# Optimization experiments

Hardware: AMD Instinct MI355X
Metric: run time of the kernel (lower is better)

Reference implementation:

```python
import jax, jax.numpy as jnp
import numpy as np

# Dims: batch B, seq L, embed D, router hidden H, num_blocks NB, top_k K
B, L, D, H, NB, K = 8, 4096, 1024, 64, 16, 2
TEMP = 2.0          # current_temperature buffer (init 2.0), clamp(min=0.1) inert
LN_EPS = 1e-5


def setup_inputs() -> dict:
    key = jax.random.key(0)
    k_x, k_w1, k_w2 = jax.random.split(key, 3)
    return {
        "x": jax.random.normal(k_x, (B, L, D), dtype=jnp.float32),
        "ln_gamma": jnp.ones((D,), dtype=jnp.float32),
        "ln_beta": jnp.zeros((D,), dtype=jnp.float32),
        "W1": jax.random.normal(k_w1, (D, H), dtype=jnp.float32) / np.sqrt(D).astype(np.float32),
        "W2": jax.random.normal(k_w2, (H, NB), dtype=jnp.float32) / np.sqrt(H).astype(np.float32),
    }


def reference(x, ln_gamma, ln_beta, W1, W2):
    # gate: LayerNorm -> Linear(no bias) -> GELU(exact) -> Linear(no bias)
    mu = jnp.mean(x, axis=-1, keepdims=True)
    var = jnp.mean(jnp.square(x - mu), axis=-1, keepdims=True)
    xn = (x - mu) * jax.lax.rsqrt(var + LN_EPS) * ln_gamma + ln_beta
    h = jax.nn.gelu(xn @ W1, approximate=False)          # (B, L, H)
    logits = (h @ W2) / TEMP                              # (B, L, NB)

    probs = jax.nn.softmax(logits, axis=-1)               # (B, L, NB)
    top_probs, indices = jax.lax.top_k(probs, K)          # (B, L, K) each
    weights = top_probs / (jnp.sum(top_probs, axis=-1, keepdims=True) + 1e-8)

    # load-balancing aux loss: f = fraction of assignments per block (detached),
    # P = mean router prob per block
    counts = jnp.zeros((NB,), dtype=probs.dtype).at[indices.reshape(-1)].add(1.0)
    f = jax.lax.stop_gradient(counts) / (B * L * K + 1e-8)
    P = jnp.mean(probs, axis=(0, 1))                      # (NB,)
    aux_loss = NB * jnp.sum(f * P)

    return probs, indices, aux_loss, weights
```

## Files before the change

### kernel.cpp

```cpp
#include <hip/hip_runtime.h>
#include <math.h>

typedef __attribute__((ext_vector_type(8))) short short8;
typedef __attribute__((ext_vector_type(4))) float f32x4;

#define NTOK 32768
#define DDIM 1024
#define HDIM 64
#define NB 16
#define LN_EPS 1e-5f

#define IDX_OFF ((size_t)NTOK * NB)
#define AUX_OFF (IDX_OFF + (size_t)NTOK * 2)
#define WT_OFF  (AUX_OFF + 1)

#define CS_F   64
#define BP_F   4352
#define PART_F 102656

__device__ __forceinline__ short8 as_s8(uint4 u) {
    union { uint4 u; short8 s; } x; x.u = u; return x.s;
}

__device__ __forceinline__ f32x4 ntload4(const float* p) {
    return __builtin_nontemporal_load((const f32x4*)p);
}

__device__ __forceinline__ void gld16(const unsigned int* g, float* l) {
    __builtin_amdgcn_global_load_lds(
        (const __attribute__((address_space(1))) void*)g,
        (__attribute__((address_space(3))) void*)l, 16, 0, 0);
}

__global__ void pack_kernel(const float* __restrict__ W1,
                            const float* __restrict__ gamma,
                            const float* __restrict__ beta,
                            float* __restrict__ ws) {
    __shared__ float sg[4][64];
    __shared__ float sb[4][64];
    const int s = blockIdx.x;
    const int t = threadIdx.x;

    {
        const int j = t & 63, p = t >> 6;
        float ag = 0.f, ab = 0.f;
        for (int kk = 0; kk < 8; ++kk) {
            const int k = s * 32 + p * 8 + kk;
            const float w = W1[k * HDIM + j];
            ag += gamma[k] * w;
            ab += beta[k] * w;
        }
        sg[p][j] = ag;
        sb[p][j] = ab;
    }

    {
        unsigned int* bp = (unsigned int*)(ws + BP_F);
        const int n = t >> 6;
        const int l = t & 63;
        const int q = l >> 4, c = l & 15;
        const int col = n * 16 + c;
        unsigned int uh[8], um[8], ul[8];
#pragma unroll
        for (int j = 0; j < 8; ++j) {
            const int k = s * 32 + q * 8 + j;
            const float w = gamma[k] * W1[k * HDIM + col];
            const unsigned int hb = __float_as_uint(w) & 0xFFFF0000u;
            const float r = w - __uint_as_float(hb);
            const unsigned int mb = __float_as_uint(r) & 0xFFFF0000u;
            const float r2 = r - __uint_as_float(mb);
            const unsigned int lb = __float_as_uint(r2) & 0xFFFF0000u;
            uh[j] = hb >> 16; um[j] = mb >> 16; ul[j] = lb >> 16;
        }
        const int base = ((s * 4 + n) * 64 + l) * 4;
#pragma unroll
        for (int d = 0; d < 4; ++d) {
            bp[base + d]         = uh[2 * d] | (uh[2 * d + 1] << 16);
            bp[32768 + base + d] = um[2 * d] | (um[2 * d + 1] << 16);
            bp[65536 + base + d] = ul[2 * d] | (ul[2 * d + 1] << 16);
        }
    }
    __syncthreads();
    if (t < 64) {
        atomicAdd(&ws[CS_F + t],      sg[0][t] + sg[1][t] + sg[2][t] + sg[3][t]);
        atomicAdd(&ws[CS_F + 64 + t], sb[0][t] + sb[1][t] + sb[2][t] + sb[3][t]);
    }
}

__device__ __forceinline__ void split8(const f32x4 a0, const f32x4 a1,
                                       short8& AH, short8& AM, short8& AL,
                                       float& s1, float& s2) {
    const float v[8] = {a0.x, a0.y, a0.z, a0.w, a1.x, a1.y, a1.z, a1.w};
    unsigned int ph[4], pm[4], pl[4];
#pragma unroll
    for (int d = 0; d < 4; ++d) {
        const float v0 = v[2 * d], v1 = v[2 * d + 1];
        const unsigned int h0 = __float_as_uint(v0) & 0xFFFF0000u;
        const unsigned int h1 = __float_as_uint(v1) & 0xFFFF0000u;
        const float r0 = v0 - __uint_as_float(h0);
        const float r1 = v1 - __uint_as_float(h1);
        const unsigned int m0 = __float_as_uint(r0) & 0xFFFF0000u;
        const unsigned int m1 = __float_as_uint(r1) & 0xFFFF0000u;
        const float q0 = r0 - __uint_as_float(m0);
        const float q1 = r1 - __uint_as_float(m1);
        ph[d] = (h0 >> 16) | h1;
        pm[d] = (m0 >> 16) | m1;
        pl[d] = (__float_as_uint(q0) >> 16) | (__float_as_uint(q1) & 0xFFFF0000u);
        s1 += v0 + v1;
        s2 = fmaf(v0, v0, fmaf(v1, v1, s2));
    }
    AH = as_s8(make_uint4(ph[0], ph[1], ph[2], ph[3]));
    AM = as_s8(make_uint4(pm[0], pm[1], pm[2], pm[3]));
    AL = as_s8(make_uint4(pl[0], pl[1], pl[2], pl[3]));
}

#define MFMA6(ACC, AH, AM, AL, BH, BM, BL)                                        \
    ACC = __builtin_amdgcn_mfma_f32_16x16x32_bf16(AH, as_s8(BH), ACC, 0, 0, 0);   \
    ACC = __builtin_amdgcn_mfma_f32_16x16x32_bf16(AH, as_s8(BM), ACC, 0, 0, 0);   \
    ACC = __builtin_amdgcn_mfma_f32_16x16x32_bf16(AM, as_s8(BH), ACC, 0, 0, 0);   \
    ACC = __builtin_amdgcn_mfma_f32_16x16x32_bf16(AH, as_s8(BL), ACC, 0, 0, 0);   \
    ACC = __builtin_amdgcn_mfma_f32_16x16x32_bf16(AM, as_s8(BM), ACC, 0, 0, 0);   \
    ACC = __builtin_amdgcn_mfma_f32_16x16x32_bf16(AL, as_s8(BH), ACC, 0, 0, 0);

#define STEP(S, CUR, NXT, DOSTAGE)                                               \
    {                                                                            \
        if (DOSTAGE) {                                                           \
            _Pragma("unroll")                                                    \
            for (int i = 0; i < 3; ++i) {                                        \
                const int idx = wv * 3 + i;                                      \
                const int term = idx >> 2, nn = idx & 3;                         \
                gld16(bp + term * 32768 + ((S) + 1) * 1024 + nn * 256 + lane * 4,\
                      (NXT) + term * 1024 + nn * 256);                           \
            }                                                                    \
        }                                                                        \
        const int off = (((S) + 2) & 31) * 32;                                   \
        const f32x4 p00 = ntload4(xr0 + off), p01 = ntload4(xr0 + off + 4);      \
        short8 AH0, AM0, AL0;                                                    \
        split8(a00, a01, AH0, AM0, AL0, s1a, s2a);                               \
        _Pragma("unroll")                                                        \
        for (int n = 0; n < 4; ++n) {                                            \
            const uint4 bh = *(const uint4*)((CUR) + n * 256 + lane * 4);        \
            const uint4 bm = *(const uint4*)((CUR) + 1024 + n * 256 + lane * 4); \
            const uint4 bl = *(const uint4*)((CUR) + 2048 + n * 256 + lane * 4); \
            MFMA6(acc[n], AH0, AM0, AL0, bh, bm, bl);                            \
        }                                                                        \
        a00 = b00; a01 = b01; b00 = p00; b01 = p01;                              \
        __syncthreads();                                                         \
    }

__global__ __launch_bounds__(256, 2)
void router_main(const float* __restrict__ x,
                 const float* __restrict__ ws_ro,
                 const unsigned int* __restrict__ bp,
                 const float* __restrict__ W2,
                 float* __restrict__ part,
                 float* __restrict__ out) {
    __shared__ __align__(16) float smem[10320];
    float* bstage = smem;
    float* hlds   = smem + 6144;
    float* cntl   = smem + 10304;
    float* w2l    = smem;
    float* llds   = smem + 1024;

    const int t    = threadIdx.x;
    const int wv   = t >> 6;
    const int lane = t & 63;
    const int q = lane >> 4, c = lane & 15;
    const int tok0 = blockIdx.x * 64;
    const int tokw = tok0 + wv * 16;

    if (t < 16) cntl[t] = 0.f;

    float csg[4], csb[4];
#pragma unroll
    for (int n = 0; n < 4; ++n) {
        csg[n] = ws_ro[CS_F + n * 16 + c];
        csb[n] = ws_ro[CS_F + 64 + n * 16 + c];
    }

    const float* xr0 = x + (size_t)(tokw + c) * DDIM + q * 8;

    float* const bufA = bstage;
    float* const bufB = bstage + 3072;

    {
#pragma unroll
        for (int i = 0; i < 3; ++i) {
            const int idx = wv * 3 + i;
            const int term = idx >> 2, nn = idx & 3;
            gld16(bp + term * 32768 + nn * 256 + lane * 4,
                  bufA + term * 1024 + nn * 256);
        }
    }

    f32x4 acc[4] = {{0.f,0.f,0.f,0.f},{0.f,0.f,0.f,0.f},{0.f,0.f,0.f,0.f},{0.f,0.f,0.f,0.f}};
    float s1a = 0.f, s2a = 0.f;

    f32x4 a00 = ntload4(xr0),      a01 = ntload4(xr0 + 4);
    f32x4 b00 = ntload4(xr0 + 32), b01 = ntload4(xr0 + 36);

    __syncthreads();

#pragma unroll 1
    for (int s2i = 0; s2i < 16; ++s2i) {
        const int s = s2i * 2;
        STEP(s,     bufA, bufB, 1)
        STEP(s + 1, bufB, bufA, (s2i < 15))
    }

    s1a += __shfl_xor(s1a, 16, 64); s1a += __shfl_xor(s1a, 32, 64);
    s2a += __shfl_xor(s2a, 16, 64); s2a += __shfl_xor(s2a, 32, 64);

    *(float4*)(w2l + t * 4) = *(const float4*)(W2 + t * 4);

    {
        float* hw = hlds + wv * 1040;
#pragma unroll
        for (int r = 0; r < 4; ++r) {
            const int tt = q * 4 + r;
            const float S1A = __shfl(s1a, tt, 64), S2A = __shfl(s2a, tt, 64);
            const float muA = S1A * (1.0f / 1024.0f);
            const float rsA = 1.0f / sqrtf(S2A * (1.0f / 1024.0f) - muA * muA + LN_EPS);
#pragma unroll
            for (int n = 0; n < 4; ++n) {
                const float preA = rsA * (acc[n][r] - muA * csg[n]) + csb[n];
                hw[tt * 65 + n * 16 + c] =
                    0.5f * preA * (1.0f + erff(preA * 0.70710678118654752f));
            }
        }
    }
    __syncthreads();

    {
        const int m2 = t >> 2, o = (t & 3) * 4;
        const float* hrow = hlds + (m2 >> 4) * 1040 + (m2 & 15) * 65;
        f32x4 L0 = {0.f, 0.f, 0.f, 0.f};
#pragma unroll 8
        for (int j = 0; j < 64; ++j) {
            L0 += *(const f32x4*)(w2l + j * 16 + o) * hrow[j];
        }
        *(f32x4*)(llds + m2 * 20 + o) = L0 * 0.5f;
    }
    __syncthreads();

    if (t < 64) {
        float p[16];
        float mx = -1e30f;
#pragma unroll
        for (int i = 0; i < NB; ++i) { p[i] = llds[t * 20 + i]; mx = fmaxf(mx, p[i]); }
        float ssum = 0.f;
#pragma unroll
        for (int i = 0; i < NB; ++i) { p[i] = expf(p[i] - mx); ssum += p[i]; }
        const float inv = 1.0f / ssum;
#pragma unroll
        for (int i = 0; i < NB; ++i) { p[i] *= inv; llds[t * 20 + i] = p[i]; }

        float* po = out + (size_t)(tok0 + t) * NB;
#pragma unroll
        for (int u = 0; u < 4; ++u) {
            float4 v; v.x = p[u*4]; v.y = p[u*4+1]; v.z = p[u*4+2]; v.w = p[u*4+3];
            *(float4*)(po + u * 4) = v;
        }

        float b0 = -1.f, b1 = -1.f;
        int i0 = 0, i1 = 0;
#pragma unroll
        for (int i = 0; i < NB; ++i) {
            if (p[i] > b0)      { b1 = b0; i1 = i0; b0 = p[i]; i0 = i; }
            else if (p[i] > b1) { b1 = p[i]; i1 = i; }
        }
        const float wsum = b0 + b1 + 1e-8f;
        out[IDX_OFF + (size_t)(tok0 + t) * 2]     = (float)i0;
        out[IDX_OFF + (size_t)(tok0 + t) * 2 + 1] = (float)i1;
        out[WT_OFF + (size_t)(tok0 + t) * 2]      = b0 / wsum;
        out[WT_OFF + (size_t)(tok0 + t) * 2 + 1]  = b1 / wsum;
        atomicAdd(&cntl[i0], 1.0f);
        atomicAdd(&cntl[i1], 1.0f);
    }
    __syncthreads();

    if (t < 16) {
        float ps = 0.f;
        for (int m = 0; m < 64; ++m) ps += llds[m * 20 + t];
        part[(size_t)blockIdx.x * 32 + t]      = cntl[t];
        part[(size_t)blockIdx.x * 32 + 16 + t] = ps;
    }
}

__global__ void aux_kernel(const float* __restrict__ part,
                           float* __restrict__ gacc,
                           float* __restrict__ out) {
    __shared__ float red[8][32];
    __shared__ float flag;
    const int t = threadIdx.x;
    const int b = blockIdx.x;
    const int i = t & 31, rr = t >> 5;
    const int r0 = b * 16 + rr;
    red[rr][i] = part[(size_t)r0 * 32 + i] + part[(size_t)(r0 + 8) * 32 + i];
    __syncthreads();
    if (t < 32) {
        float tot = 0.f;
#pragma unroll
        for (int p = 0; p < 8; ++p) tot += red[p][t];
        atomicAdd(&gacc[t], tot);
    }
    __syncthreads();
    if (t == 0) {
        __threadfence();
        const unsigned int old = atomicAdd((unsigned int*)(gacc + 32), 1u);
        flag = (old == 31u) ? 1.f : 0.f;
    }
    __syncthreads();
    if (flag != 0.f) {
        if (t < 32) red[0][t] = atomicAdd(&gacc[t], 0.0f);
        __syncthreads();
        if (t == 0) {
            float a = 0.f;
            for (int k = 0; k < NB; ++k) {
                const float f = red[0][k] / (65536.0f + 1e-8f);
                const float P = red[0][16 + k] * (1.0f / 32768.0f);
                a += f * P;
            }
            out[AUX_OFF] = 16.0f * a;
        }
    }
}

extern "C" void kernel_launch(void* const* d_in, const int* in_sizes, int n_in,
                              void* d_out, int out_size, void* d_ws, size_t ws_size,
                              hipStream_t stream) {
    const float* x     = (const float*)d_in[0];
    const float* gamma = (const float*)d_in[1];
    const float* beta  = (const float*)d_in[2];
    const float* W1    = (const float*)d_in[3];
    const float* W2    = (const float*)d_in[4];
    float* out = (float*)d_out;
    float* ws  = (float*)d_ws;

    (void)hipMemsetAsync(ws, 0, 192 * sizeof(float), stream);
    pack_kernel<<<32, 256, 0, stream>>>(W1, gamma, beta, ws);
    router_main<<<NTOK / 64, 256, 0, stream>>>(x, ws, (const unsigned int*)(ws + BP_F),
                                               W2, ws + PART_F, out);
    aux_kernel<<<32, 256, 0, stream>>>(ws + PART_F, ws, out);
}
```

Baseline: 227.6 us.

## Stage x through LDS with async loads, double-buffer 64-wide chunks, 128-token blocks

The main router kernel now fetches the x tiles with global_load_lds into double-buffered shared memory alongside the split W1 operands, instead of nontemporal register loads. Each barrier now covers two K-steps instead of one. Waits are explicit vmcnt counts so the next chunk's loads overlap the current MFMAs. Blocks grow to 512 threads and 128 tokens, and the aux reduction grid is halved to match. This trades more LDS per block (about 112KB, which may limit residency) for fewer barriers and better latency hiding.

```diff
diff --git a/kernel.cpp b/kernel.cpp
--- a/kernel.cpp
+++ b/kernel.cpp
@@ -22,11 +22,7 @@
     union { uint4 u; short8 s; } x; x.u = u; return x.s;
 }
 
-__device__ __forceinline__ f32x4 ntload4(const float* p) {
-    return __builtin_nontemporal_load((const f32x4*)p);
-}
-
-__device__ __forceinline__ void gld16(const unsigned int* g, float* l) {
+__device__ __forceinline__ void gld16(const void* g, float* l) {
     __builtin_amdgcn_global_load_lds(
         (const __attribute__((address_space(1))) void*)g,
         (__attribute__((address_space(3))) void*)l, 16, 0, 0);
@@ -122,54 +118,37 @@
     ACC = __builtin_amdgcn_mfma_f32_16x16x32_bf16(AM, as_s8(BM), ACC, 0, 0, 0);   \
     ACC = __builtin_amdgcn_mfma_f32_16x16x32_bf16(AL, as_s8(BH), ACC, 0, 0, 0);
 
-#define STEP(S, CUR, NXT, DOSTAGE)                                               \
-    {                                                                            \
-        if (DOSTAGE) {                                                           \
-            _Pragma("unroll")                                                    \
-            for (int i = 0; i < 3; ++i) {                                        \
-                const int idx = wv * 3 + i;                                      \
-                const int term = idx >> 2, nn = idx & 3;                         \
-                gld16(bp + term * 32768 + ((S) + 1) * 1024 + nn * 256 + lane * 4,\
-                      (NXT) + term * 1024 + nn * 256);                           \
-            }                                                                    \
-        }                                                                        \
-        const int off = (((S) + 2) & 31) * 32;                                   \
-        const f32x4 p00 = ntload4(xr0 + off), p01 = ntload4(xr0 + off + 4);      \
-        short8 AH0, AM0, AL0;                                                    \
-        split8(a00, a01, AH0, AM0, AL0, s1a, s2a);                               \
-        _Pragma("unroll")                                                        \
-        for (int n = 0; n < 4; ++n) {                                            \
-            const uint4 bh = *(const uint4*)((CUR) + n * 256 + lane * 4);        \
-            const uint4 bm = *(const uint4*)((CUR) + 1024 + n * 256 + lane * 4); \
-            const uint4 bl = *(const uint4*)((CUR) + 2048 + n * 256 + lane * 4); \
-            MFMA6(acc[n], AH0, AM0, AL0, bh, bm, bl);                            \
-        }                                                                        \
-        a00 = b00; a01 = b01; b00 = p00; b01 = p01;                              \
-        __syncthreads();                                                         \
-    }
-
-__global__ __launch_bounds__(256, 2)
+#define WAITV(N)                                                   \
+    asm volatile("s_waitcnt vmcnt(" #N ")" ::: "memory");          \
+    __builtin_amdgcn_sched_barrier(0)
+
+#define BARRIER_PUB()                                              \
+    asm volatile("s_waitcnt vmcnt(4) lgkmcnt(0)" ::: "memory");    \
+    __builtin_amdgcn_s_barrier();                                  \
+    asm volatile("" ::: "memory");                                 \
+    __builtin_amdgcn_sched_barrier(0)
+
+#define A_F 0
+#define B_F 16384
+__global__ __launch_bounds__(512, 2)
 void router_main(const float* __restrict__ x,
                  const float* __restrict__ ws_ro,
                  const unsigned int* __restrict__ bp,
                  const float* __restrict__ W2,
                  float* __restrict__ part,
                  float* __restrict__ out) {
-    __shared__ __align__(16) float smem[10320];
-    float* bstage = smem;
-    float* hlds   = smem + 6144;
-    float* cntl   = smem + 10304;
-    float* w2l    = smem;
-    float* llds   = smem + 1024;
+    __shared__ __align__(16) float smem[28672];
+    float* hlds = smem;
+    float* w2l  = smem + 8320;
+    float* llds = smem + 9344;
+    float* cntl = smem + 11904;
 
     const int t    = threadIdx.x;
     const int wv   = t >> 6;
     const int lane = t & 63;
     const int q = lane >> 4, c = lane & 15;
-    const int tok0 = blockIdx.x * 64;
+    const int tok0 = blockIdx.x * 128;
     const int tokw = tok0 + wv * 16;
-
-    if (t < 16) cntl[t] = 0.f;
 
     float csg[4], csb[4];
 #pragma unroll
@@ -178,40 +157,78 @@
         csb[n] = ws_ro[CS_F + 64 + n * 16 + c];
     }
 
-    const float* xr0 = x + (size_t)(tokw + c) * DDIM + q * 8;
-
-    float* const bufA = bstage;
-    float* const bufB = bstage + 3072;
-
-    {
-#pragma unroll
-        for (int i = 0; i < 3; ++i) {
-            const int idx = wv * 3 + i;
-            const int term = idx >> 2, nn = idx & 3;
-            gld16(bp + term * 32768 + nn * 256 + lane * 4,
-                  bufA + term * 1024 + nn * 256);
-        }
-    }
+    const int bidx0 = wv * 3;
+    const float* xsrc = x + (size_t)(tokw + c) * DDIM + q * 8;
+
+#define STAGE_B(CI)                                                              \
+    {                                                                            \
+        float* dst = smem + B_F + ((CI) & 1) * 6144;                             \
+        _Pragma("unroll")                                                        \
+        for (int i = 0; i < 3; ++i) {                                            \
+            const int idx = bidx0 + i;                                           \
+            const int st = (idx >= 12) ? 1 : 0;                                  \
+            const int rem = idx - st * 12;                                       \
+            const int term = rem >> 2, n = rem & 3;                              \
+            gld16(bp + term * 32768 + (2 * (CI) + st) * 1024 + n * 256 + lane*4, \
+                  dst + st * 3072 + term * 1024 + n * 256);                      \
+        }                                                                        \
+    }
+#define STAGE_A(CI)                                                              \
+    {                                                                            \
+        float* dst = smem + A_F + ((CI) & 1) * 8192 + wv * 1024;                 \
+        const float* src = xsrc + (2 * (CI)) * 32;                               \
+        _Pragma("unroll")                                                        \
+        for (int j = 0; j < 4; ++j)                                              \
+            gld16(src + (j >> 1) * 32 + (j & 1) * 4, dst + j * 256);             \
+    }
+
+    STAGE_B(0)
+    STAGE_A(0)
+    asm volatile("s_waitcnt vmcnt(4)" ::: "memory");
+    __builtin_amdgcn_s_barrier();
+    asm volatile("" ::: "memory");
+    __builtin_amdgcn_sched_barrier(0);
 
     f32x4 acc[4] = {{0.f,0.f,0.f,0.f},{0.f,0.f,0.f,0.f},{0.f,0.f,0.f,0.f},{0.f,0.f,0.f,0.f}};
     float s1a = 0.f, s2a = 0.f;
 
-    f32x4 a00 = ntload4(xr0),      a01 = ntload4(xr0 + 4);
-    f32x4 b00 = ntload4(xr0 + 32), b01 = ntload4(xr0 + 36);
-
-    __syncthreads();
-
 #pragma unroll 1
-    for (int s2i = 0; s2i < 16; ++s2i) {
-        const int s = s2i * 2;
-        STEP(s,     bufA, bufB, 1)
-        STEP(s + 1, bufB, bufA, (s2i < 15))
-    }
+    for (int ci = 0; ci < 16; ++ci) {
+        if (ci < 15) {
+            STAGE_B(ci + 1)
+            STAGE_A(ci + 1)
+            WAITV(7);
+        } else {
+            WAITV(0);
+        }
+        const float* Ab = smem + A_F + (ci & 1) * 8192 + wv * 1024;
+        const float* Bb = smem + B_F + (ci & 1) * 6144;
+#pragma unroll
+        for (int st = 0; st < 2; ++st) {
+            const f32x4 a00 = *(const f32x4*)(Ab + st * 512 + lane * 4);
+            const f32x4 a01 = *(const f32x4*)(Ab + st * 512 + 256 + lane * 4);
+            short8 AH0, AM0, AL0;
+            split8(a00, a01, AH0, AM0, AL0, s1a, s2a);
+            const float* Bs = Bb + st * 3072;
+#pragma unroll
+            for (int n = 0; n < 4; ++n) {
+                const uint4 bh = *(const uint4*)(Bs + n * 256 + lane * 4);
+                const uint4 bm = *(const uint4*)(Bs + 1024 + n * 256 + lane * 4);
+                const uint4 bl = *(const uint4*)(Bs + 2048 + n * 256 + lane * 4);
+                MFMA6(acc[n], AH0, AM0, AL0, bh, bm, bl);
+            }
+        }
+        if (ci < 15) {
+            BARRIER_PUB();
+        }
+    }
+    __syncthreads();
 
     s1a += __shfl_xor(s1a, 16, 64); s1a += __shfl_xor(s1a, 32, 64);
     s2a += __shfl_xor(s2a, 16, 64); s2a += __shfl_xor(s2a, 32, 64);
 
-    *(float4*)(w2l + t * 4) = *(const float4*)(W2 + t * 4);
+    if (t < 16) cntl[t] = 0.f;
+    if (t < 256) *(float4*)(w2l + t * 4) = *(const float4*)(W2 + t * 4);
 
     {
         float* hw = hlds + wv * 1040;
@@ -243,7 +260,7 @@
     }
     __syncthreads();
 
-    if (t < 64) {
+    if (t < 128) {
         float p[16];
         float mx = -1e30f;
 #pragma unroll
@@ -281,7 +298,7 @@
 
     if (t < 16) {
         float ps = 0.f;
-        for (int m = 0; m < 64; ++m) ps += llds[m * 20 + t];
+        for (int m = 0; m < 128; ++m) ps += llds[m * 20 + t];
         part[(size_t)blockIdx.x * 32 + t]      = cntl[t];
         part[(size_t)blockIdx.x * 32 + 16 + t] = ps;
     }
@@ -308,7 +325,7 @@
     if (t == 0) {
         __threadfence();
         const unsigned int old = atomicAdd((unsigned int*)(gacc + 32), 1u);
-        flag = (old == 31u) ? 1.f : 0.f;
+        flag = (old == 15u) ? 1.f : 0.f;
     }
     __syncthreads();
     if (flag != 0.f) {
@@ -339,7 +356,7 @@
 
     (void)hipMemsetAsync(ws, 0, 192 * sizeof(float), stream);
     pack_kernel<<<32, 256, 0, stream>>>(W1, gamma, beta, ws);
-    router_main<<<NTOK / 64, 256, 0, stream>>>(x, ws, (const unsigned int*)(ws + BP_F),
-                                               W2, ws + PART_F, out);
-    aux_kernel<<<32, 256, 0, stream>>>(ws + PART_F, ws, out);
-}
+    router_main<<<NTOK / 128, 512, 0, stream>>>(x, ws, (const unsigned int*)(ws + BP_F),
+                                                W2, ws + PART_F, out);
+    aux_kernel<<<16, 256, 0, stream>>>(ws + PART_F, ws, out);
+}
```

Result: no change. 227.6 us (+0.0%).

## Split K across waves in router GEMM and reduce partials via LDS

Applied to the files above, without the earlier changes.

The main kernel now has each of the four waves handle a quarter of the 1024-wide reduction dimension for all 64 tokens, instead of each wave streaming the full row for 16 tokens. The double-buffered LDS staging and per-step barriers are gone: B fragments load directly from global memory, and the partial accumulators and LayerNorm sums are combined through LDS after the loop. The aux reduction is simplified to per-block global atomics plus a single-block finalize kernel. In exchange the kernel uses more LDS and registers (16 accumulators per lane), which may lower occupancy, and it does more global atomics.

```diff
diff --git a/kernel.cpp b/kernel.cpp
--- a/kernel.cpp
+++ b/kernel.cpp
@@ -16,7 +16,6 @@
 
 #define CS_F   64
 #define BP_F   4352
-#define PART_F 102656
 
 __device__ __forceinline__ short8 as_s8(uint4 u) {
     union { uint4 u; short8 s; } x; x.u = u; return x.s;
@@ -24,12 +23,6 @@
 
 __device__ __forceinline__ f32x4 ntload4(const float* p) {
     return __builtin_nontemporal_load((const f32x4*)p);
-}
-
-__device__ __forceinline__ void gld16(const unsigned int* g, float* l) {
-    __builtin_amdgcn_global_load_lds(
-        (const __attribute__((address_space(1))) void*)g,
-        (__attribute__((address_space(3))) void*)l, 16, 0, 0);
 }
 
 __global__ void pack_kernel(const float* __restrict__ W1,
@@ -122,122 +115,134 @@
     ACC = __builtin_amdgcn_mfma_f32_16x16x32_bf16(AM, as_s8(BM), ACC, 0, 0, 0);   \
     ACC = __builtin_amdgcn_mfma_f32_16x16x32_bf16(AL, as_s8(BH), ACC, 0, 0, 0);
 
-#define STEP(S, CUR, NXT, DOSTAGE)                                               \
-    {                                                                            \
-        if (DOSTAGE) {                                                           \
-            _Pragma("unroll")                                                    \
-            for (int i = 0; i < 3; ++i) {                                        \
-                const int idx = wv * 3 + i;                                      \
-                const int term = idx >> 2, nn = idx & 3;                         \
-                gld16(bp + term * 32768 + ((S) + 1) * 1024 + nn * 256 + lane * 4,\
-                      (NXT) + term * 1024 + nn * 256);                           \
-            }                                                                    \
-        }                                                                        \
-        const int off = (((S) + 2) & 31) * 32;                                   \
-        const f32x4 p00 = ntload4(xr0 + off), p01 = ntload4(xr0 + off + 4);      \
-        short8 AH0, AM0, AL0;                                                    \
-        split8(a00, a01, AH0, AM0, AL0, s1a, s2a);                               \
-        _Pragma("unroll")                                                        \
-        for (int n = 0; n < 4; ++n) {                                            \
-            const uint4 bh = *(const uint4*)((CUR) + n * 256 + lane * 4);        \
-            const uint4 bm = *(const uint4*)((CUR) + 1024 + n * 256 + lane * 4); \
-            const uint4 bl = *(const uint4*)((CUR) + 2048 + n * 256 + lane * 4); \
-            MFMA6(acc[n], AH0, AM0, AL0, bh, bm, bl);                            \
-        }                                                                        \
-        a00 = b00; a01 = b01; b00 = p00; b01 = p01;                              \
-        __syncthreads();                                                         \
-    }
-
 __global__ __launch_bounds__(256, 2)
 void router_main(const float* __restrict__ x,
                  const float* __restrict__ ws_ro,
                  const unsigned int* __restrict__ bp,
                  const float* __restrict__ W2,
-                 float* __restrict__ part,
+                 float* __restrict__ gacc,
                  float* __restrict__ out) {
-    __shared__ __align__(16) float smem[10320];
-    float* bstage = smem;
-    float* hlds   = smem + 6144;
-    float* cntl   = smem + 10304;
-    float* w2l    = smem;
-    float* llds   = smem + 1024;
+    __shared__ __align__(16) float smem[18064];
+    float* csgl = smem + 17408;
+    float* csbl = smem + 17472;
+    float* s1l  = smem + 17536;
+    float* s2l  = smem + 17792;
+    float* cntl = smem + 18048;
+    float* llds = smem + 4352;
 
     const int t    = threadIdx.x;
     const int wv   = t >> 6;
     const int lane = t & 63;
     const int q = lane >> 4, c = lane & 15;
     const int tok0 = blockIdx.x * 64;
-    const int tokw = tok0 + wv * 16;
-
+
+    if (t < 64) csgl[t] = ws_ro[CS_F + t];
+    else if (t < 128) csbl[t - 64] = ws_ro[CS_F + 64 + (t - 64)];
     if (t < 16) cntl[t] = 0.f;
 
-    float csg[4], csb[4];
-#pragma unroll
-    for (int n = 0; n < 4; ++n) {
-        csg[n] = ws_ro[CS_F + n * 16 + c];
-        csb[n] = ws_ro[CS_F + 64 + n * 16 + c];
-    }
-
-    const float* xr0 = x + (size_t)(tokw + c) * DDIM + q * 8;
-
-    float* const bufA = bstage;
-    float* const bufB = bstage + 3072;
-
-    {
-#pragma unroll
-        for (int i = 0; i < 3; ++i) {
-            const int idx = wv * 3 + i;
-            const int term = idx >> 2, nn = idx & 3;
-            gld16(bp + term * 32768 + nn * 256 + lane * 4,
-                  bufA + term * 1024 + nn * 256);
-        }
-    }
-
-    f32x4 acc[4] = {{0.f,0.f,0.f,0.f},{0.f,0.f,0.f,0.f},{0.f,0.f,0.f,0.f},{0.f,0.f,0.f,0.f}};
-    float s1a = 0.f, s2a = 0.f;
-
-    f32x4 a00 = ntload4(xr0),      a01 = ntload4(xr0 + 4);
-    f32x4 b00 = ntload4(xr0 + 32), b01 = ntload4(xr0 + 36);
-
-    __syncthreads();
+    const float* xg[4];
+#pragma unroll
+    for (int g = 0; g < 4; ++g)
+        xg[g] = x + (size_t)(tok0 + g * 16 + c) * DDIM + wv * 256 + q * 8;
+    const unsigned int* bpl = bp + lane * 4;
+
+    f32x4 acc[4][4];
+#pragma unroll
+    for (int g = 0; g < 4; ++g)
+#pragma unroll
+        for (int n = 0; n < 4; ++n) acc[g][n] = (f32x4){0.f, 0.f, 0.f, 0.f};
+    float s1g[4] = {0.f, 0.f, 0.f, 0.f};
+    float s2g[4] = {0.f, 0.f, 0.f, 0.f};
 
 #pragma unroll 1
-    for (int s2i = 0; s2i < 16; ++s2i) {
-        const int s = s2i * 2;
-        STEP(s,     bufA, bufB, 1)
-        STEP(s + 1, bufB, bufA, (s2i < 15))
-    }
-
-    s1a += __shfl_xor(s1a, 16, 64); s1a += __shfl_xor(s1a, 32, 64);
-    s2a += __shfl_xor(s2a, 16, 64); s2a += __shfl_xor(s2a, 32, 64);
-
-    *(float4*)(w2l + t * 4) = *(const float4*)(W2 + t * 4);
-
-    {
-        float* hw = hlds + wv * 1040;
-#pragma unroll
-        for (int r = 0; r < 4; ++r) {
-            const int tt = q * 4 + r;
-            const float S1A = __shfl(s1a, tt, 64), S2A = __shfl(s2a, tt, 64);
-            const float muA = S1A * (1.0f / 1024.0f);
-            const float rsA = 1.0f / sqrtf(S2A * (1.0f / 1024.0f) - muA * muA + LN_EPS);
+    for (int it = 0; it < 8; ++it) {
+        const int s = wv * 8 + it;
+        f32x4 a0v[4], a1v[4];
+#pragma unroll
+        for (int g = 0; g < 4; ++g) {
+            a0v[g] = ntload4(xg[g] + it * 32);
+            a1v[g] = ntload4(xg[g] + it * 32 + 4);
+        }
+        uint4 bh[4], bm[4], bl[4];
+#pragma unroll
+        for (int n = 0; n < 4; ++n) {
+            bh[n] = *(const uint4*)(bpl + (s * 4 + n) * 256);
+            bm[n] = *(const uint4*)(bpl + 32768 + (s * 4 + n) * 256);
+            bl[n] = *(const uint4*)(bpl + 65536 + (s * 4 + n) * 256);
+        }
+#pragma unroll
+        for (int g = 0; g < 4; ++g) {
+            short8 AH, AM, AL;
+            split8(a0v[g], a1v[g], AH, AM, AL, s1g[g], s2g[g]);
 #pragma unroll
             for (int n = 0; n < 4; ++n) {
-                const float preA = rsA * (acc[n][r] - muA * csg[n]) + csb[n];
-                hw[tt * 65 + n * 16 + c] =
-                    0.5f * preA * (1.0f + erff(preA * 0.70710678118654752f));
+                MFMA6(acc[g][n], AH, AM, AL, bh[n], bm[n], bl[n]);
             }
         }
     }
+
+#pragma unroll
+    for (int g = 0; g < 4; ++g) {
+        s1g[g] += __shfl_xor(s1g[g], 16, 64); s1g[g] += __shfl_xor(s1g[g], 32, 64);
+        s2g[g] += __shfl_xor(s2g[g], 16, 64); s2g[g] += __shfl_xor(s2g[g], 32, 64);
+    }
+    if (lane < 16) {
+#pragma unroll
+        for (int g = 0; g < 4; ++g) {
+            s1l[wv * 64 + g * 16 + c] = s1g[g];
+            s2l[wv * 64 + g * 16 + c] = s2g[g];
+        }
+    }
+
+    {
+        float* yw = smem + wv * 4352;
+#pragma unroll
+        for (int g = 0; g < 4; ++g)
+#pragma unroll
+            for (int n = 0; n < 4; ++n)
+#pragma unroll
+                for (int r = 0; r < 4; ++r)
+                    yw[(g * 16 + q * 4 + r) * 68 + n * 16 + c] = acc[g][n][r];
+    }
+    __syncthreads();
+
+    {
+        const int m = t >> 2, cb = (t & 3) * 16;
+        const float S1 = s1l[m] + s1l[64 + m] + s1l[128 + m] + s1l[192 + m];
+        const float S2 = s2l[m] + s2l[64 + m] + s2l[128 + m] + s2l[192 + m];
+        const float mu   = S1 * (1.0f / 1024.0f);
+        const float var  = S2 * (1.0f / 1024.0f) - mu * mu;
+        const float rstd = 1.0f / sqrtf(var + LN_EPS);
+        f32x4 yv[4];
+#pragma unroll
+        for (int k = 0; k < 4; ++k) {
+            const int off = m * 68 + cb + k * 4;
+            yv[k] = *(const f32x4*)(smem + off)
+                  + *(const f32x4*)(smem + 4352 + off)
+                  + *(const f32x4*)(smem + 8704 + off)
+                  + *(const f32x4*)(smem + 13056 + off);
+        }
+#pragma unroll
+        for (int k = 0; k < 4; ++k)
+#pragma unroll
+            for (int e = 0; e < 4; ++e) {
+                const int col = cb + k * 4 + e;
+                const float pre = rstd * (yv[k][e] - mu * csgl[col]) + csbl[col];
+                yv[k][e] = 0.5f * pre * (1.0f + erff(pre * 0.70710678118654752f));
+            }
+#pragma unroll
+        for (int k = 0; k < 4; ++k)
+            *(f32x4*)(smem + m * 68 + cb + k * 4) = yv[k];
+    }
     __syncthreads();
 
     {
         const int m2 = t >> 2, o = (t & 3) * 4;
-        const float* hrow = hlds + (m2 >> 4) * 1040 + (m2 & 15) * 65;
+        const float* hrow = smem + m2 * 68;
         f32x4 L0 = {0.f, 0.f, 0.f, 0.f};
 #pragma unroll 8
         for (int j = 0; j < 64; ++j) {
-            L0 += *(const f32x4*)(w2l + j * 16 + o) * hrow[j];
+            L0 += *(const f32x4*)(W2 + j * 16 + o) * hrow[j];
         }
         *(f32x4*)(llds + m2 * 20 + o) = L0 * 0.5f;
     }
@@ -282,47 +287,25 @@
     if (t < 16) {
         float ps = 0.f;
         for (int m = 0; m < 64; ++m) ps += llds[m * 20 + t];
-        part[(size_t)blockIdx.x * 32 + t]      = cntl[t];
-        part[(size_t)blockIdx.x * 32 + 16 + t] = ps;
-    }
-}
-
-__global__ void aux_kernel(const float* __restrict__ part,
-                           float* __restrict__ gacc,
+        atomicAdd(&gacc[t], cntl[t]);
+        atomicAdd(&gacc[16 + t], ps);
+    }
+}
+
+__global__ void aux_kernel(float* __restrict__ gacc,
                            float* __restrict__ out) {
-    __shared__ float red[8][32];
-    __shared__ float flag;
+    __shared__ float red[32];
     const int t = threadIdx.x;
-    const int b = blockIdx.x;
-    const int i = t & 31, rr = t >> 5;
-    const int r0 = b * 16 + rr;
-    red[rr][i] = part[(size_t)r0 * 32 + i] + part[(size_t)(r0 + 8) * 32 + i];
-    __syncthreads();
-    if (t < 32) {
-        float tot = 0.f;
-#pragma unroll
-        for (int p = 0; p < 8; ++p) tot += red[p][t];
-        atomicAdd(&gacc[t], tot);
-    }
+    if (t < 32) red[t] = atomicAdd(&gacc[t], 0.0f);
     __syncthreads();
     if (t == 0) {
-        __threadfence();
-        const unsigned int old = atomicAdd((unsigned int*)(gacc + 32), 1u);
-        flag = (old == 31u) ? 1.f : 0.f;
-    }
-    __syncthreads();
-    if (flag != 0.f) {
-        if (t < 32) red[0][t] = atomicAdd(&gacc[t], 0.0f);
-        __syncthreads();
-        if (t == 0) {
-            float a = 0.f;
-            for (int k = 0; k < NB; ++k) {
-                const float f = red[0][k] / (65536.0f + 1e-8f);
-                const float P = red[0][16 + k] * (1.0f / 32768.0f);
-                a += f * P;
-            }
-            out[AUX_OFF] = 16.0f * a;
-        }
+        float a = 0.f;
+        for (int k = 0; k < NB; ++k) {
+            const float f = red[k] / (65536.0f + 1e-8f);
+            const float P = red[16 + k] * (1.0f / 32768.0f);
+            a += f * P;
+        }
+        out[AUX_OFF] = 16.0f * a;
     }
 }
 
@@ -340,6 +323,6 @@
     (void)hipMemsetAsync(ws, 0, 192 * sizeof(float), stream);
     pack_kernel<<<32, 256, 0, stream>>>(W1, gamma, beta, ws);
     router_main<<<NTOK / 64, 256, 0, stream>>>(x, ws, (const unsigned int*)(ws + BP_F),
-                                               W2, ws + PART_F, out);
-    aux_kernel<<<32, 256, 0, stream>>>(ws + PART_F, ws, out);
-}
+                                               W2, ws, out);
+    aux_kernel<<<1, 64, 0, stream>>>(ws, out);
+}
```

Result: faster. 221.1 us (-2.9%).
